# Kernel tuning notes

Hardware: AMD Instinct MI355X
Metric: run time of the kernel (lower is better)

## Reference

```python
import jax, jax.numpy as jnp
import numpy as np

N_VARS = 28
HID = 64
BATCH = 32768
BN_EPS = 1e-5


def _lin_init(key, fan_in, shape):
    bound = 1.0 / np.sqrt(fan_in)
    return jax.random.uniform(key, shape, minval=-bound, maxval=bound, dtype=jnp.float32)


def setup_inputs() -> dict:
    key = jax.random.key(0)
    ks = jax.random.split(key, 8)
    n, h = N_VARS, HID
    X = jax.random.normal(ks[0], (BATCH, n), dtype=jnp.float32)
    W_logits = jax.random.uniform(ks[1], (n, n), minval=-0.01, maxval=0.01, dtype=jnp.float32)
    # per-mechanism (grouped) weights, stacked on leading mechanism axis n
    W1 = _lin_init(ks[2], n, (n, h, n)); b1 = _lin_init(ks[3], n, (n, h))
    W2 = _lin_init(ks[4], h, (n, h, h)); b2 = _lin_init(ks[5], h, (n, h))
    W3 = _lin_init(ks[6], h, (n, 1, h)); b3 = _lin_init(ks[7], h, (n, 1))
    gamma1 = jnp.ones((n, h)); beta1 = jnp.zeros((n, h))
    gamma2 = jnp.ones((n, h)); beta2 = jnp.zeros((n, h))
    return {"X": X, "W_logits": W_logits,
            "W1": W1, "b1": b1, "gamma1": gamma1, "beta1": beta1,
            "W2": W2, "b2": b2, "gamma2": gamma2, "beta2": beta2,
            "W3": W3, "b3": b3}


def _bn(x, gamma, beta):
    # x: [n, B, h]; batch stats over B (training-mode BatchNorm1d, biased var)
    m = x.mean(axis=1, keepdims=True)
    v = ((x - m) ** 2).mean(axis=1, keepdims=True)
    return gamma[:, None, :] * (x - m) * jax.lax.rsqrt(v + BN_EPS) + beta[:, None, :]


def reference(X, W_logits, W1, b1, gamma1, beta1, W2, b2, gamma2, beta2, W3, b3):
    n = W_logits.shape[0]
    # adjacency: sigmoid with zeroed diagonal
    W = jax.nn.sigmoid(W_logits) * (1.0 - jnp.eye(n, dtype=W_logits.dtype))
    # fuse the parent mask into the first layer's weights: one grouped GEMM
    # instead of n_vars separate masked matmuls
    W1_eff = W1 * W[:, None, :]                               # [n, h, n]
    h1 = jnp.einsum('bd,nhd->nbh', X, W1_eff) + b1[:, None, :]  # [n, B, h]
    a1 = jax.nn.gelu(_bn(h1, gamma1, beta1), approximate=False)
    h2 = jnp.einsum('nbh,ngh->nbg', a1, W2) + b2[:, None, :]
    a2 = jax.nn.gelu(_bn(h2, gamma2, beta2), approximate=False)
    out = jnp.einsum('nbh,noh->nbo', a2, W3) + b3[:, None, :]   # [n, B, 1]
    X_hat = out[:, :, 0].T                                     # [B, n]
    return (X_hat, W)
```

## Files before the change

### kernel.cpp

```cpp
#include <hip/hip_runtime.h>
#include <hip/hip_bf16.h>
#include <math.h>

typedef float  f4 __attribute__((ext_vector_type(4)));
typedef short  s8 __attribute__((ext_vector_type(8)));
typedef short  s4 __attribute__((ext_vector_type(4)));

#define NV 28
#define NB 32768
#define BN_EPS 1e-5f

#define SUM2_OFF   0
#define SSQ2_OFF   1792
#define BIAS1_OFF  3584
#define PART_OFF   9772
#define BF_BASE_F  217644
#define W2B_OFF_S  57344
#define XBF_OFF_S  172032

__device__ __forceinline__ float gelu_f(float x) {
    float x2 = x * x;
    float z  = x * __builtin_fmaf(x2, -0.10294324f, -2.3022082f);
    float t  = __builtin_amdgcn_exp2f(z);
    return x * __builtin_amdgcn_rcpf(1.0f + t);
}
__device__ __forceinline__ unsigned short f2bf(float x) {
    unsigned u = __builtin_bit_cast(unsigned, x);
    return (unsigned short)((u + 0x7fffu + ((u >> 16) & 1u)) >> 16);
}
__device__ __forceinline__ float row16_sum(float v) {
    int x;
    x = __builtin_amdgcn_update_dpp(0, __builtin_bit_cast(int, v), 0xB1, 0xF, 0xF, true);
    v += __builtin_bit_cast(float, x);
    x = __builtin_amdgcn_update_dpp(0, __builtin_bit_cast(int, v), 0x4E, 0xF, 0xF, true);
    v += __builtin_bit_cast(float, x);
    x = __builtin_amdgcn_update_dpp(0, __builtin_bit_cast(int, v), 0x124, 0xF, 0xF, true);
    v += __builtin_bit_cast(float, x);
    x = __builtin_amdgcn_update_dpp(0, __builtin_bit_cast(int, v), 0x128, 0xF, 0xF, true);
    v += __builtin_bit_cast(float, x);
    return v;
}
__device__ __forceinline__ float quad4_sum(float v) {
    int x;
    x = __builtin_amdgcn_update_dpp(0, __builtin_bit_cast(int, v), 0xB1, 0xF, 0xF, true);
    v += __builtin_bit_cast(float, x);
    x = __builtin_amdgcn_update_dpp(0, __builtin_bit_cast(int, v), 0x4E, 0xF, 0xF, true);
    v += __builtin_bit_cast(float, x);
    return v;
}

__global__ __launch_bounds__(256) void k_xstats(const float* __restrict__ X,
                                                float* __restrict__ ws) {
    __shared__ float sx[128 * 28];
    const int tid = threadIdx.x;
    float acc[4] = {0.f, 0.f, 0.f, 0.f};
    int* xb = (int*)((short*)(ws + BF_BASE_F) + XBF_OFF_S);
    for (int c = 0; c < 4; ++c) {
        const int rowbase = blockIdx.x * 512 + c * 128;
        {
            const f4* src = (const f4*)(X + (size_t)rowbase * 28);
            f4* dst = (f4*)sx;
            for (int i = tid; i < 128 * 28 / 4; i += 256) dst[i] = src[i];
        }
        __syncthreads();
        for (int j = tid; j < 128 * 16; j += 256) {
            int row = j >> 4, cc = j & 15;
            float lo = (2 * cc     < 28) ? sx[row * 28 + 2 * cc]     : 0.0f;
            float hi = (2 * cc + 1 < 28) ? sx[row * 28 + 2 * cc + 1] : 0.0f;
            xb[(size_t)(rowbase + row) * 16 + cc] =
                (int)f2bf(lo) | ((int)f2bf(hi) << 16);
        }
#pragma unroll
        for (int s = 0; s < 4; ++s) {
            int slot = tid + s * 256;
            if (slot < 812) {
                float a = acc[s];
                if (slot < 28) {
                    for (int r = 0; r < 128; ++r) a += sx[r * 28 + slot];
                } else {
                    int p = slot - 28;
                    int d = p / 28, e = p % 28;
                    for (int r = 0; r < 128; ++r) a += sx[r * 28 + d] * sx[r * 28 + e];
                }
                acc[s] = a;
            }
        }
        __syncthreads();
    }
#pragma unroll
    for (int s = 0; s < 4; ++s) {
        int slot = tid + s * 256;
        if (slot < 812) ws[PART_OFF + blockIdx.x * 812 + slot] = acc[s];
    }
}

__global__ __launch_bounds__(256) void k_fold1(const float* __restrict__ Wlog,
                                               const float* __restrict__ W1,
                                               const float* __restrict__ g1,
                                               const float* __restrict__ be1,
                                               const float* __restrict__ W2,
                                               float* __restrict__ ws,
                                               float* __restrict__ out_w) {
    __shared__ float sstat[812];
    __shared__ float wrow[28];
    __shared__ float C[784];
    __shared__ float w1e_s[64 * 28];
    const int n = blockIdx.x, t = threadIdx.x;

    for (int s = t; s < 812; s += 256) {
        float a = 0.0f;
#pragma unroll 16
        for (int p = 0; p < 64; ++p) a += ws[PART_OFF + p * 812 + s];
        sstat[s] = a;
    }
    if (t < 64) {
        ws[SUM2_OFF + n * 64 + t] = 0.0f;
        ws[SSQ2_OFF + n * 64 + t] = 0.0f;
    }
    __syncthreads();

    if (t < 28) {
        float w = 1.0f / (1.0f + expf(-Wlog[n * 28 + t]));
        if (t == n) w = 0.0f;
        wrow[t] = w;
        out_w[n * 28 + t] = w;
    }
    for (int i = t; i < 784; i += 256) {
        int d = i / 28, e = i % 28;
        C[i] = sstat[28 + i] * (1.0f / 32768.0f)
             - sstat[d] * (1.0f / 32768.0f) * sstat[e] * (1.0f / 32768.0f);
    }
    __syncthreads();
    for (int i = t; i < 1792; i += 256) {
        int d = i % 28;
        w1e_s[i] = W1[(size_t)n * 1792 + i] * wrow[d];
    }
    __syncthreads();

    const int h = t >> 2, j = t & 3;
    const float* we = &w1e_s[h * 28];
    float var_p = 0.0f, dot_p = 0.0f;
#pragma unroll
    for (int k = 0; k < 7; ++k) {
        int d = 7 * j + k;
        float inner = 0.0f;
#pragma unroll
        for (int e = 0; e < 28; ++e) inner = __builtin_fmaf(C[d * 28 + e], we[e], inner);
        float wd = we[d];
        var_p = __builtin_fmaf(inner, wd, var_p);
        dot_p = __builtin_fmaf(wd, sstat[d] * (1.0f / 32768.0f), dot_p);
    }
    float var  = quad4_sum(var_p);
    float dotm = quad4_sum(dot_p);
    float scale = g1[n * 64 + h] * rsqrtf(fmaxf(var, 0.0f) + BN_EPS);
    if (j == 0)
        ws[BIAS1_OFF + n * 64 + h] = be1[n * 64 + h] - dotm * scale;

    short* bfbase = (short*)(ws + BF_BASE_F);
    {
        short* w1f = bfbase + (size_t)(n * 64 + h) * 32;
        s8 pk;
#pragma unroll
        for (int k = 0; k < 8; ++k) {
            int d = 8 * j + k;
            pk[k] = (short)f2bf(d < 28 ? we[d] * scale : 0.0f);
        }
        *(s8*)&w1f[8 * j] = pk;
    }
    {
        const float* w2src = W2 + (size_t)n * 4096 + t * 16;
        short* w2d = bfbase + W2B_OFF_S + (size_t)n * 4096 + t * 16;
        s8 a, b;
#pragma unroll
        for (int k = 0; k < 8; ++k) a[k] = (short)f2bf(w2src[k]);
#pragma unroll
        for (int k = 0; k < 8; ++k) b[k] = (short)f2bf(w2src[8 + k]);
        *(s8*)&w2d[0] = a;
        *(s8*)&w2d[8] = b;
    }
}

__global__ __launch_bounds__(256, 4) void k_pass1(float* __restrict__ ws) {
    __shared__ __align__(16) short sW1[64 * 40];
    __shared__ __align__(16) short sW2[64 * 72];
    __shared__ __align__(16) short sA1[8 * 16 * 72];
    __shared__ float sP1[4][64], sP2[4][64];

    const int n = blockIdx.x >> 7;
    const int blk = blockIdx.x & 127;
    const int tid = threadIdx.x;
    const int wave = tid >> 6;
    const int lane = tid & 63;
    const int m = lane & 15;
    const int q = lane >> 4;

    const short* bfbase = (const short*)(ws + BF_BASE_F);
    const short* w1g = bfbase + (size_t)n * 64 * 32;
    const short* w2g = bfbase + W2B_OFF_S + (size_t)n * 64 * 64;
    const short* xbf = bfbase + XBF_OFF_S;
    {
        int r = tid >> 2, c = tid & 3;
        *(s8*)&sW1[r * 40 + c * 8] = *(const s8*)&w1g[r * 32 + c * 8];
#pragma unroll
        for (int k = 0; k < 2; ++k) {
            int i2 = tid + k * 256;
            int r2 = i2 >> 3, c2 = i2 & 7;
            *(s8*)&sW2[r2 * 72 + c2 * 8] = *(const s8*)&w2g[r2 * 64 + c2 * 8];
        }
    }
    __syncthreads();

    const float* bias1 = ws + BIAS1_OFF + n * 64;
    short* myA1a = &sA1[(wave * 2 + 0) * 16 * 72];
    short* myA1b = &sA1[(wave * 2 + 1) * 16 * 72];
    float s1[16], s2v[16];
#pragma unroll
    for (int i = 0; i < 16; ++i) { s1[i] = 0.0f; s2v[i] = 0.0f; }

#pragma unroll
    for (int it = 0; it < 2; ++it) {
        const int row0 = blk * 256 + it * 128 + wave * 32;
        s8 xfa = *(const s8*)&xbf[(size_t)(row0 + m) * 32 + 8 * q];
        s8 xfb = *(const s8*)&xbf[(size_t)(row0 + 16 + m) * 32 + 8 * q];

        f4 acc1a[4], acc1b[4];
#pragma unroll
        for (int t = 0; t < 4; ++t) {
            s8 wf = *(const s8*)&sW1[(16 * t + m) * 40 + q * 8];
            acc1a[t] = __builtin_amdgcn_mfma_f32_16x16x32_bf16(wf, xfa, (f4){0.f, 0.f, 0.f, 0.f}, 0, 0, 0);
            acc1b[t] = __builtin_amdgcn_mfma_f32_16x16x32_bf16(wf, xfb, (f4){0.f, 0.f, 0.f, 0.f}, 0, 0, 0);
        }
#pragma unroll
        for (int t = 0; t < 4; ++t) {
            f4 bv = *(const f4*)&bias1[16 * t + 4 * q];
            s4 pa, pb;
#pragma unroll
            for (int r = 0; r < 4; ++r) {
                pa[r] = (short)f2bf(gelu_f(acc1a[t][r] + bv[r]));
                pb[r] = (short)f2bf(gelu_f(acc1b[t][r] + bv[r]));
            }
            *(s4*)&myA1a[m * 72 + 16 * t + 4 * q] = pa;
            *(s4*)&myA1b[m * 72 + 16 * t + 4 * q] = pb;
        }
        s8 af0a = *(const s8*)&myA1a[m * 72 + 8 * q];
        s8 af1a = *(const s8*)&myA1a[m * 72 + 32 + 8 * q];
        s8 af0b = *(const s8*)&myA1b[m * 72 + 8 * q];
        s8 af1b = *(const s8*)&myA1b[m * 72 + 32 + 8 * q];
#pragma unroll
        for (int u = 0; u < 4; ++u) {
            s8 w0 = *(const s8*)&sW2[(16 * u + m) * 72 + 8 * q];
            s8 w1 = *(const s8*)&sW2[(16 * u + m) * 72 + 32 + 8 * q];
            f4 aa = (f4){0.f, 0.f, 0.f, 0.f};
            f4 ab = (f4){0.f, 0.f, 0.f, 0.f};
            aa = __builtin_amdgcn_mfma_f32_16x16x32_bf16(w0, af0a, aa, 0, 0, 0);
            ab = __builtin_amdgcn_mfma_f32_16x16x32_bf16(w0, af0b, ab, 0, 0, 0);
            aa = __builtin_amdgcn_mfma_f32_16x16x32_bf16(w1, af1a, aa, 0, 0, 0);
            ab = __builtin_amdgcn_mfma_f32_16x16x32_bf16(w1, af1b, ab, 0, 0, 0);
#pragma unroll
            for (int r = 0; r < 4; ++r) {
                s1[u * 4 + r]  += aa[r] + ab[r];
                s2v[u * 4 + r] = __builtin_fmaf(aa[r], aa[r], s2v[u * 4 + r]);
                s2v[u * 4 + r] = __builtin_fmaf(ab[r], ab[r], s2v[u * 4 + r]);
            }
        }
    }
#pragma unroll
    for (int u = 0; u < 4; ++u) {
#pragma unroll
        for (int r = 0; r < 4; ++r) {
            float t1 = row16_sum(s1[u * 4 + r]);
            float t2 = row16_sum(s2v[u * 4 + r]);
            if (m == 0) {
                sP1[wave][16 * u + 4 * q + r] = t1;
                sP2[wave][16 * u + 4 * q + r] = t2;
            }
        }
    }
    __syncthreads();
    if (tid < 64) {
        float a = sP1[0][tid] + sP1[1][tid] + sP1[2][tid] + sP1[3][tid];
        float b = sP2[0][tid] + sP2[1][tid] + sP2[2][tid] + sP2[3][tid];
        atomicAdd(&ws[SUM2_OFF + n * 64 + tid], a);
        atomicAdd(&ws[SSQ2_OFF + n * 64 + tid], b);
    }
}

__global__ __launch_bounds__(256, 4) void k_pass2(const float* __restrict__ g2,
                                                  const float* __restrict__ be2,
                                                  const float* __restrict__ W3,
                                                  const float* __restrict__ b3,
                                                  float* __restrict__ ws,
                                                  float* __restrict__ out) {
    __shared__ __align__(16) short sW1[64 * 40];
    __shared__ __align__(16) short sW2[64 * 72];
    __shared__ __align__(16) short sA1[8 * 16 * 72];
    __shared__ float sSc[64], sSh[64], sW3v[64];

    const int n = blockIdx.x >> 7;
    const int blk = blockIdx.x & 127;
    const int tid = threadIdx.x;
    const int wave = tid >> 6;
    const int lane = tid & 63;
    const int m = lane & 15;
    const int q = lane >> 4;

    const short* bfbase = (const short*)(ws + BF_BASE_F);
    const short* w1g = bfbase + (size_t)n * 64 * 32;
    const short* w2g = bfbase + W2B_OFF_S + (size_t)n * 64 * 64;
    const short* xbf = bfbase + XBF_OFF_S;
    {
        int r = tid >> 2, c = tid & 3;
        *(s8*)&sW1[r * 40 + c * 8] = *(const s8*)&w1g[r * 32 + c * 8];
#pragma unroll
        for (int k = 0; k < 2; ++k) {
            int i2 = tid + k * 256;
            int r2 = i2 >> 3, c2 = i2 & 7;
            *(s8*)&sW2[r2 * 72 + c2 * 8] = *(const s8*)&w2g[r2 * 64 + c2 * 8];
        }
        if (tid < 64) {
            float mean = ws[SUM2_OFF + n * 64 + tid] * (1.0f / 32768.0f);
            float var  = ws[SSQ2_OFF + n * 64 + tid] * (1.0f / 32768.0f) - mean * mean;
            float sc = g2[n * 64 + tid] * rsqrtf(fmaxf(var, 0.0f) + BN_EPS);
            sSc[tid]  = sc;
            sSh[tid]  = be2[n * 64 + tid] - mean * sc;
            sW3v[tid] = W3[n * 64 + tid];
        }
    }
    __syncthreads();

    const float* bias1 = ws + BIAS1_OFF + n * 64;
    const float b3n = b3[n];
    short* myA1a = &sA1[(wave * 2 + 0) * 16 * 72];
    short* myA1b = &sA1[(wave * 2 + 1) * 16 * 72];

#pragma unroll
    for (int it = 0; it < 2; ++it) {
        const int row0 = blk * 256 + it * 128 + wave * 32;
        s8 xfa = *(const s8*)&xbf[(size_t)(row0 + m) * 32 + 8 * q];
        s8 xfb = *(const s8*)&xbf[(size_t)(row0 + 16 + m) * 32 + 8 * q];

        f4 acc1a[4], acc1b[4];
#pragma unroll
        for (int t = 0; t < 4; ++t) {
            s8 wf = *(const s8*)&sW1[(16 * t + m) * 40 + q * 8];
            acc1a[t] = __builtin_amdgcn_mfma_f32_16x16x32_bf16(wf, xfa, (f4){0.f, 0.f, 0.f, 0.f}, 0, 0, 0);
            acc1b[t] = __builtin_amdgcn_mfma_f32_16x16x32_bf16(wf, xfb, (f4){0.f, 0.f, 0.f, 0.f}, 0, 0, 0);
        }
#pragma unroll
        for (int t = 0; t < 4; ++t) {
            f4 bv = *(const f4*)&bias1[16 * t + 4 * q];
            s4 pa, pb;
#pragma unroll
            for (int r = 0; r < 4; ++r) {
                pa[r] = (short)f2bf(gelu_f(acc1a[t][r] + bv[r]));
                pb[r] = (short)f2bf(gelu_f(acc1b[t][r] + bv[r]));
            }
            *(s4*)&myA1a[m * 72 + 16 * t + 4 * q] = pa;
            *(s4*)&myA1b[m * 72 + 16 * t + 4 * q] = pb;
        }
        s8 af0a = *(const s8*)&myA1a[m * 72 + 8 * q];
        s8 af1a = *(const s8*)&myA1a[m * 72 + 32 + 8 * q];
        s8 af0b = *(const s8*)&myA1b[m * 72 + 8 * q];
        s8 af1b = *(const s8*)&myA1b[m * 72 + 32 + 8 * q];
        float pa = 0.0f, pb = 0.0f;
#pragma unroll
        for (int u = 0; u < 4; ++u) {
            s8 w0 = *(const s8*)&sW2[(16 * u + m) * 72 + 8 * q];
            s8 w1 = *(const s8*)&sW2[(16 * u + m) * 72 + 32 + 8 * q];
            f4 aa = (f4){0.f, 0.f, 0.f, 0.f};
            f4 ab = (f4){0.f, 0.f, 0.f, 0.f};
            aa = __builtin_amdgcn_mfma_f32_16x16x32_bf16(w0, af0a, aa, 0, 0, 0);
            ab = __builtin_amdgcn_mfma_f32_16x16x32_bf16(w0, af0b, ab, 0, 0, 0);
            aa = __builtin_amdgcn_mfma_f32_16x16x32_bf16(w1, af1a, aa, 0, 0, 0);
            ab = __builtin_amdgcn_mfma_f32_16x16x32_bf16(w1, af1b, ab, 0, 0, 0);
            f4 scv = *(const f4*)&sSc[16 * u + 4 * q];
            f4 shv = *(const f4*)&sSh[16 * u + 4 * q];
            f4 w3v = *(const f4*)&sW3v[16 * u + 4 * q];
#pragma unroll
            for (int r = 0; r < 4; ++r) {
                float va = __builtin_fmaf(aa[r], scv[r], shv[r]);
                float vb = __builtin_fmaf(ab[r], scv[r], shv[r]);
                pa = __builtin_fmaf(gelu_f(va), w3v[r], pa);
                pb = __builtin_fmaf(gelu_f(vb), w3v[r], pb);
            }
        }
        pa += __shfl_xor(pa, 16);  pa += __shfl_xor(pa, 32);
        pb += __shfl_xor(pb, 16);  pb += __shfl_xor(pb, 32);
        if (q == 0) {
            out[(size_t)(row0 + m) * 28 + n]      = pa + b3n;
            out[(size_t)(row0 + 16 + m) * 28 + n] = pb + b3n;
        }
    }
}

extern "C" void kernel_launch(void* const* d_in, const int* in_sizes, int n_in,
                              void* d_out, int out_size, void* d_ws, size_t ws_size,
                              hipStream_t stream) {
    const float* X   = (const float*)d_in[0];
    const float* Wl  = (const float*)d_in[1];
    const float* W1  = (const float*)d_in[2];
    const float* g1  = (const float*)d_in[4];
    const float* be1 = (const float*)d_in[5];
    const float* W2  = (const float*)d_in[6];
    const float* g2  = (const float*)d_in[8];
    const float* be2 = (const float*)d_in[9];
    const float* W3  = (const float*)d_in[10];
    const float* b3  = (const float*)d_in[11];
    float* out = (float*)d_out;
    float* ws  = (float*)d_ws;

    k_xstats<<<dim3(64), dim3(256), 0, stream>>>(X, ws);
    k_fold1<<<dim3(28), dim3(256), 0, stream>>>(Wl, W1, g1, be1, W2, ws, out + 917504);
    k_pass1<<<dim3(28 * 128), dim3(256), 0, stream>>>(ws);
    k_pass2<<<dim3(28 * 128), dim3(256), 0, stream>>>(g2, be2, W3, b3, ws, out);
}
```

Before: 215.2 us.

## Store layer-2 preactivations in bf16 to skip recompute in second pass

Result: faster. 187.4 us (-12.9%).

```diff
diff --git a/kernel.cpp b/kernel.cpp
--- a/kernel.cpp
+++ b/kernel.cpp
@@ -9,14 +9,18 @@
 #define NV 28
 #define NB 32768
 #define BN_EPS 1e-5f
+#define NSLOT 434
 
 #define SUM2_OFF   0
 #define SSQ2_OFF   1792
 #define BIAS1_OFF  3584
-#define PART_OFF   9772
-#define BF_BASE_F  217644
+#define REDU_OFF   5376
+#define PART_OFF   5824
+#define BF_BASE_F  116992
 #define W2B_OFF_S  57344
 #define XBF_OFF_S  172032
+#define H2_BYTE_OFF 2909184ull
+#define H2_BYTES    117440512ull
 
 __device__ __forceinline__ float gelu_f(float x) {
     float x2 = x * x;
@@ -28,6 +32,9 @@
     unsigned u = __builtin_bit_cast(unsigned, x);
     return (unsigned short)((u + 0x7fffu + ((u >> 16) & 1u)) >> 16);
 }
+__device__ __forceinline__ float bf2f(short s) {
+    return __builtin_bit_cast(float, ((int)(unsigned short)s) << 16);
+}
 __device__ __forceinline__ float row16_sum(float v) {
     int x;
     x = __builtin_amdgcn_update_dpp(0, __builtin_bit_cast(int, v), 0xB1, 0xF, 0xF, true);
@@ -53,44 +60,42 @@
                                                 float* __restrict__ ws) {
     __shared__ float sx[128 * 28];
     const int tid = threadIdx.x;
-    float acc[4] = {0.f, 0.f, 0.f, 0.f};
+    const int rowbase = blockIdx.x * 128;
+    {
+        const f4* src = (const f4*)(X + (size_t)rowbase * 28);
+        f4* dst = (f4*)sx;
+        for (int i = tid; i < 128 * 28 / 4; i += 256) dst[i] = src[i];
+    }
+    __syncthreads();
     int* xb = (int*)((short*)(ws + BF_BASE_F) + XBF_OFF_S);
-    for (int c = 0; c < 4; ++c) {
-        const int rowbase = blockIdx.x * 512 + c * 128;
-        {
-            const f4* src = (const f4*)(X + (size_t)rowbase * 28);
-            f4* dst = (f4*)sx;
-            for (int i = tid; i < 128 * 28 / 4; i += 256) dst[i] = src[i];
-        }
-        __syncthreads();
-        for (int j = tid; j < 128 * 16; j += 256) {
-            int row = j >> 4, cc = j & 15;
-            float lo = (2 * cc     < 28) ? sx[row * 28 + 2 * cc]     : 0.0f;
-            float hi = (2 * cc + 1 < 28) ? sx[row * 28 + 2 * cc + 1] : 0.0f;
-            xb[(size_t)(rowbase + row) * 16 + cc] =
-                (int)f2bf(lo) | ((int)f2bf(hi) << 16);
-        }
-#pragma unroll
-        for (int s = 0; s < 4; ++s) {
-            int slot = tid + s * 256;
-            if (slot < 812) {
-                float a = acc[s];
-                if (slot < 28) {
-                    for (int r = 0; r < 128; ++r) a += sx[r * 28 + slot];
-                } else {
-                    int p = slot - 28;
-                    int d = p / 28, e = p % 28;
-                    for (int r = 0; r < 128; ++r) a += sx[r * 28 + d] * sx[r * 28 + e];
-                }
-                acc[s] = a;
-            }
-        }
-        __syncthreads();
-    }
-#pragma unroll
-    for (int s = 0; s < 4; ++s) {
-        int slot = tid + s * 256;
-        if (slot < 812) ws[PART_OFF + blockIdx.x * 812 + slot] = acc[s];
+    for (int j = tid; j < 128 * 16; j += 256) {
+        int row = j >> 4, cc = j & 15;
+        float lo = (2 * cc     < 28) ? sx[row * 28 + 2 * cc]     : 0.0f;
+        float hi = (2 * cc + 1 < 28) ? sx[row * 28 + 2 * cc + 1] : 0.0f;
+        xb[(size_t)(rowbase + row) * 16 + cc] = (int)f2bf(lo) | ((int)f2bf(hi) << 16);
+    }
+    for (int s = tid; s < NSLOT; s += 256) {
+        float a = 0.0f;
+        if (s < 28) {
+            for (int r = 0; r < 128; ++r) a += sx[r * 28 + s];
+        } else {
+            int p = s - 28, d = 0, rem = 28;
+            while (p >= rem) { p -= rem; ++d; --rem; }
+            int e = d + p;
+            for (int r = 0; r < 128; ++r)
+                a = __builtin_fmaf(sx[r * 28 + d], sx[r * 28 + e], a);
+        }
+        ws[PART_OFF + blockIdx.x * NSLOT + s] = a;
+    }
+}
+
+__global__ __launch_bounds__(256) void k_reduce(float* __restrict__ ws) {
+    int s = blockIdx.x * 256 + threadIdx.x;
+    if (s < NSLOT) {
+        float a = 0.0f;
+#pragma unroll 16
+        for (int p = 0; p < 256; ++p) a += ws[PART_OFF + p * NSLOT + s];
+        ws[REDU_OFF + s] = a;
     }
 }
 
@@ -101,40 +106,31 @@
                                                const float* __restrict__ W2,
                                                float* __restrict__ ws,
                                                float* __restrict__ out_w) {
-    __shared__ float sstat[812];
-    __shared__ float wrow[28];
+    __shared__ float mu[28], wrow[28];
     __shared__ float C[784];
     __shared__ float w1e_s[64 * 28];
     const int n = blockIdx.x, t = threadIdx.x;
 
-    for (int s = t; s < 812; s += 256) {
-        float a = 0.0f;
-#pragma unroll 16
-        for (int p = 0; p < 64; ++p) a += ws[PART_OFF + p * 812 + s];
-        sstat[s] = a;
-    }
-    if (t < 64) {
-        ws[SUM2_OFF + n * 64 + t] = 0.0f;
-        ws[SSQ2_OFF + n * 64 + t] = 0.0f;
-    }
-    __syncthreads();
-
     if (t < 28) {
+        mu[t] = ws[REDU_OFF + t] * (1.0f / 32768.0f);
         float w = 1.0f / (1.0f + expf(-Wlog[n * 28 + t]));
         if (t == n) w = 0.0f;
         wrow[t] = w;
         out_w[n * 28 + t] = w;
     }
+    if (t < 64) {
+        ws[SUM2_OFF + n * 64 + t] = 0.0f;
+        ws[SSQ2_OFF + n * 64 + t] = 0.0f;
+    }
+    __syncthreads();
     for (int i = t; i < 784; i += 256) {
         int d = i / 28, e = i % 28;
-        C[i] = sstat[28 + i] * (1.0f / 32768.0f)
-             - sstat[d] * (1.0f / 32768.0f) * sstat[e] * (1.0f / 32768.0f);
-    }
-    __syncthreads();
-    for (int i = t; i < 1792; i += 256) {
-        int d = i % 28;
-        w1e_s[i] = W1[(size_t)n * 1792 + i] * wrow[d];
-    }
+        int lo = d < e ? d : e, hi = d < e ? e : d;
+        int idx = 28 + lo * 28 - (lo * (lo - 1)) / 2 + (hi - lo);
+        C[i] = ws[REDU_OFF + idx] * (1.0f / 32768.0f) - mu[d] * mu[e];
+    }
+    for (int i = t; i < 1792; i += 256)
+        w1e_s[i] = W1[(size_t)n * 1792 + i] * wrow[i % 28];
     __syncthreads();
 
     const int h = t >> 2, j = t & 3;
@@ -148,7 +144,7 @@
         for (int e = 0; e < 28; ++e) inner = __builtin_fmaf(C[d * 28 + e], we[e], inner);
         float wd = we[d];
         var_p = __builtin_fmaf(inner, wd, var_p);
-        dot_p = __builtin_fmaf(wd, sstat[d] * (1.0f / 32768.0f), dot_p);
+        dot_p = __builtin_fmaf(wd, mu[d], dot_p);
     }
     float var  = quad4_sum(var_p);
     float dotm = quad4_sum(dot_p);
@@ -180,7 +176,9 @@
     }
 }
 
-__global__ __launch_bounds__(256, 4) void k_pass1(float* __restrict__ ws) {
+template <bool STORE>
+__global__ __launch_bounds__(256, 4) void k_pass1(float* __restrict__ ws,
+                                                  short* __restrict__ h2buf) {
     __shared__ __align__(16) short sW1[64 * 40];
     __shared__ __align__(16) short sW2[64 * 72];
     __shared__ __align__(16) short sA1[8 * 16 * 72];
@@ -246,6 +244,8 @@
         s8 af1a = *(const s8*)&myA1a[m * 72 + 32 + 8 * q];
         s8 af0b = *(const s8*)&myA1b[m * 72 + 8 * q];
         s8 af1b = *(const s8*)&myA1b[m * 72 + 32 + 8 * q];
+        short* hpA = STORE ? (h2buf + ((size_t)n * NB + row0 + m) * 64) : nullptr;
+        short* hpB = STORE ? (h2buf + ((size_t)n * NB + row0 + 16 + m) * 64) : nullptr;
 #pragma unroll
         for (int u = 0; u < 4; ++u) {
             s8 w0 = *(const s8*)&sW2[(16 * u + m) * 72 + 8 * q];
@@ -256,6 +256,13 @@
             ab = __builtin_amdgcn_mfma_f32_16x16x32_bf16(w0, af0b, ab, 0, 0, 0);
             aa = __builtin_amdgcn_mfma_f32_16x16x32_bf16(w1, af1a, aa, 0, 0, 0);
             ab = __builtin_amdgcn_mfma_f32_16x16x32_bf16(w1, af1b, ab, 0, 0, 0);
+            if (STORE) {
+                s4 ha, hb;
+#pragma unroll
+                for (int r = 0; r < 4; ++r) { ha[r] = (short)f2bf(aa[r]); hb[r] = (short)f2bf(ab[r]); }
+                *(s4*)&hpA[16 * u + 4 * q] = ha;
+                *(s4*)&hpB[16 * u + 4 * q] = hb;
+            }
 #pragma unroll
             for (int r = 0; r < 4; ++r) {
                 s1[u * 4 + r]  += aa[r] + ab[r];
@@ -285,12 +292,47 @@
     }
 }
 
-__global__ __launch_bounds__(256, 4) void k_pass2(const float* __restrict__ g2,
-                                                  const float* __restrict__ be2,
-                                                  const float* __restrict__ W3,
-                                                  const float* __restrict__ b3,
-                                                  float* __restrict__ ws,
-                                                  float* __restrict__ out) {
+__global__ __launch_bounds__(256) void k_pass2s(const float* __restrict__ g2,
+                                                const float* __restrict__ be2,
+                                                const float* __restrict__ W3,
+                                                const float* __restrict__ b3,
+                                                const float* __restrict__ ws,
+                                                const short* __restrict__ h2buf,
+                                                float* __restrict__ out) {
+    __shared__ float sSc[64], sSh[64], sW3v[64];
+    const int n = blockIdx.x >> 7;
+    const int row = ((blockIdx.x & 127) << 8) + threadIdx.x;
+    if (threadIdx.x < 64) {
+        int g = threadIdx.x;
+        float mean = ws[SUM2_OFF + n * 64 + g] * (1.0f / 32768.0f);
+        float var  = ws[SSQ2_OFF + n * 64 + g] * (1.0f / 32768.0f) - mean * mean;
+        float sc = g2[n * 64 + g] * rsqrtf(fmaxf(var, 0.0f) + BN_EPS);
+        sSc[g]  = sc;
+        sSh[g]  = be2[n * 64 + g] - mean * sc;
+        sW3v[g] = W3[n * 64 + g];
+    }
+    __syncthreads();
+    const short* hp = h2buf + ((size_t)n * NB + row) * 64;
+    float p = 0.0f;
+#pragma unroll
+    for (int c = 0; c < 8; ++c) {
+        s8 hv = *(const s8*)&hp[c * 8];
+#pragma unroll
+        for (int k = 0; k < 8; ++k) {
+            int g = c * 8 + k;
+            float v = bf2f(hv[k]);
+            p = __builtin_fmaf(gelu_f(__builtin_fmaf(v, sSc[g], sSh[g])), sW3v[g], p);
+        }
+    }
+    out[(size_t)row * 28 + n] = p + b3[n];
+}
+
+__global__ __launch_bounds__(256, 4) void k_pass2r(const float* __restrict__ g2,
+                                                   const float* __restrict__ be2,
+                                                   const float* __restrict__ W3,
+                                                   const float* __restrict__ b3,
+                                                   float* __restrict__ ws,
+                                                   float* __restrict__ out) {
     __shared__ __align__(16) short sW1[64 * 40];
     __shared__ __align__(16) short sW2[64 * 72];
     __shared__ __align__(16) short sA1[8 * 16 * 72];
@@ -408,9 +450,17 @@
     const float* b3  = (const float*)d_in[11];
     float* out = (float*)d_out;
     float* ws  = (float*)d_ws;
-
-    k_xstats<<<dim3(64), dim3(256), 0, stream>>>(X, ws);
+    short* h2buf = (short*)((char*)d_ws + H2_BYTE_OFF);
+    const bool store_h2 = ws_size >= H2_BYTE_OFF + H2_BYTES;
+
+    k_xstats<<<dim3(256), dim3(256), 0, stream>>>(X, ws);
+    k_reduce<<<dim3(2), dim3(256), 0, stream>>>(ws);
     k_fold1<<<dim3(28), dim3(256), 0, stream>>>(Wl, W1, g1, be1, W2, ws, out + 917504);
-    k_pass1<<<dim3(28 * 128), dim3(256), 0, stream>>>(ws);
-    k_pass2<<<dim3(28 * 128), dim3(256), 0, stream>>>(g2, be2, W3, b3, ws, out);
-}
+    if (store_h2) {
+        k_pass1<true><<<dim3(28 * 128), dim3(256), 0, stream>>>(ws, h2buf);
+        k_pass2s<<<dim3(28 * 128), dim3(256), 0, stream>>>(g2, be2, W3, b3, ws, h2buf, out);
+    } else {
+        k_pass1<false><<<dim3(28 * 128), dim3(256), 0, stream>>>(ws, nullptr);
+        k_pass2r<<<dim3(28 * 128), dim3(256), 0, stream>>>(g2, be2, W3, b3, ws, out);
+    }
+}
```
